# Kernel optimization log

Hardware: AMD Instinct MI355X
Metric: run time of the kernel (lower is better)

Reference implementation:

```python
import jax, jax.numpy as jnp
import numpy as np

B, S, D = 2, 2048, 3584
H, KV, HD = 28, 4, 128
N_REP = H // KV          # 7
MAX_S = 2048
SCALE = HD ** -0.5
ROPE_BASE = 1_000_000.0  # Qwen2 rope theta


def _rope_tables(max_s, hd, base):
    inv = 1.0 / (base ** (np.arange(0, hd, 2, dtype=np.float32) / hd))  # [hd/2]
    ang = np.arange(max_s, dtype=np.float32)[:, None] * inv[None, :]    # [S, hd/2]
    return jnp.asarray(np.cos(ang)), jnp.asarray(np.sin(ang))


def apply_rotary(x, cos, sin):
    # x: [b, s, h, hd] with interleaved complex pairs (torch view_as_complex layout)
    xr = x[..., 0::2]
    xi = x[..., 1::2]
    cos = cos[None, :, None, :]
    sin = sin[None, :, None, :]
    yr = xr * cos - xi * sin
    yi = xr * sin + xi * cos
    return jnp.stack([yr, yi], axis=-1).reshape(x.shape)


def setup_inputs() -> dict:
    key = jax.random.key(0)
    ks = jax.random.split(key, 8)
    w = 0.02
    x = jax.random.normal(ks[0], (B, S, D), jnp.float32)
    wq_w = jax.random.normal(ks[1], (H * HD, D), jnp.float32) * w
    wq_b = jax.random.normal(ks[2], (H * HD,), jnp.float32) * w
    wk_w = jax.random.normal(ks[3], (KV * HD, D), jnp.float32) * w
    wk_b = jax.random.normal(ks[4], (KV * HD,), jnp.float32) * w
    wv_w = jax.random.normal(ks[5], (KV * HD, D), jnp.float32) * w
    wv_b = jax.random.normal(ks[6], (KV * HD,), jnp.float32) * w
    wo_w = jax.random.normal(ks[7], (D, H * HD), jnp.float32) * w
    k_cache = jnp.zeros((B, MAX_S, KV, HD), jnp.float32)
    v_cache = jnp.zeros((B, MAX_S, KV, HD), jnp.float32)
    freqs_cos, freqs_sin = _rope_tables(MAX_S, HD, ROPE_BASE)
    # causal additive mask [s, t]; large-negative instead of -inf for safe grads
    mask = jnp.triu(jnp.full((S, S), -1e9, jnp.float32), k=1)
    return {"x": x, "wq_w": wq_w, "wq_b": wq_b, "wk_w": wk_w, "wk_b": wk_b,
            "wv_w": wv_w, "wv_b": wv_b, "wo_w": wo_w,
            "k_cache": k_cache, "v_cache": v_cache,
            "freqs_cos": freqs_cos, "freqs_sin": freqs_sin,
            "mask": mask, "start_pos": 0}


def reference(x, wq_w, wq_b, wk_w, wk_b, wv_w, wv_b, wo_w,
              k_cache, v_cache, freqs_cos, freqs_sin, mask, start_pos):
    bsz, seqlen, _ = x.shape
    end_pos = start_pos + seqlen
    q = (x @ wq_w.T + wq_b).reshape(bsz, seqlen, H, HD)
    k = (x @ wk_w.T + wk_b).reshape(bsz, seqlen, KV, HD)
    v = (x @ wv_w.T + wv_b).reshape(bsz, seqlen, KV, HD)
    cos = jax.lax.dynamic_slice_in_dim(freqs_cos, start_pos, seqlen, 0)
    sin = jax.lax.dynamic_slice_in_dim(freqs_sin, start_pos, seqlen, 0)
    q = apply_rotary(q, cos, sin)
    k = apply_rotary(k, cos, sin)
    # KV-cache write
    k_cache = jax.lax.dynamic_update_slice(k_cache, k, (0, start_pos, 0, 0))
    v_cache = jax.lax.dynamic_update_slice(v_cache, v, (0, start_pos, 0, 0))
    keys = k_cache[:bsz, :end_pos]    # [b, t, kv, hd]
    values = v_cache[:bsz, :end_pos]
    # GQA: repeat_interleave kv heads to n_heads
    keys = jnp.repeat(keys, N_REP, axis=2)      # [b, t, h, hd]
    values = jnp.repeat(values, N_REP, axis=2)
    scores = jnp.einsum('bshd,bthd->bsht', q, keys) * SCALE
    scores = scores + mask[None, :, None, :]
    probs = jax.nn.softmax(scores.astype(jnp.float32), axis=-1).astype(x.dtype)
    out = jnp.einsum('bsht,bthd->bshd', probs, values)
    out = out.reshape(bsz, seqlen, H * HD)
    return out @ wo_w.T
```

## Files before the change

kernel.cpp:

```cpp
#include <hip/hip_runtime.h>
#include <hip/hip_bf16.h>

typedef __attribute__((ext_vector_type(4)))  float  f32x4;
typedef __attribute__((ext_vector_type(16))) float  f32x16;
typedef __attribute__((ext_vector_type(8)))  __bf16 bf16x8;
typedef __attribute__((ext_vector_type(4)))  __bf16 bf16x4;
typedef __attribute__((ext_vector_type(4)))  unsigned int u32x4;

constexpr int S_LEN = 2048, DMODEL = 3584, NH = 28, NKV = 4, HD = 128, NREP = 7;
constexpr float SCALE_LOG2 = 0.1275174331f;

__device__ __forceinline__ unsigned int pack2(float a, float b) {
  unsigned short ua = __builtin_bit_cast(unsigned short, (__bf16)a);
  unsigned short ub = __builtin_bit_cast(unsigned short, (__bf16)b);
  return (unsigned int)ua | ((unsigned int)ub << 16);
}

__global__ void cvt5_kernel(const float* __restrict__ s0, const float* __restrict__ s1,
                            const float* __restrict__ s2, const float* __restrict__ s3,
                            const float* __restrict__ s4,
                            __bf16* __restrict__ d0, __bf16* __restrict__ d1,
                            __bf16* __restrict__ d2, __bf16* __restrict__ d3,
                            __bf16* __restrict__ d4,
                            int n0, int n1, int n2, int n3, int* __restrict__ ctr, int total) {
  if (blockIdx.x == 0 && threadIdx.x == 0) *ctr = 0;
  for (int i = blockIdx.x * blockDim.x + threadIdx.x; i < total; i += gridDim.x * blockDim.x) {
    const float* s; __bf16* d; int j = i;
    if (j < n0) { s = s0; d = d0; }
    else { j -= n0;
      if (j < n1) { s = s1; d = d1; }
      else { j -= n1;
        if (j < n2) { s = s2; d = d2; }
        else { j -= n2;
          if (j < n3) { s = s3; d = d3; }
          else { j -= n3; s = s4; d = d4; }
        }
      }
    }
    float4 v = reinterpret_cast<const float4*>(s)[j];
    bf16x4 o;
    o[0] = (__bf16)v.x; o[1] = (__bf16)v.y; o[2] = (__bf16)v.z; o[3] = (__bf16)v.w;
    reinterpret_cast<bf16x4*>(d)[j] = o;
  }
}

#define GLDS16(gsrc, ldst)                                                              \
  __builtin_amdgcn_global_load_lds((const __attribute__((address_space(1))) void*)(gsrc),\
                                   (__attribute__((address_space(3))) void*)(ldst), 16, 0, 0)

template <int MODE>
__global__ __launch_bounds__(512, 4) void gemm256(
    const __bf16* __restrict__ A, const __bf16* __restrict__ Bw,
    const float* __restrict__ bias, void* __restrict__ Cout,
    int M, int N, int K,
    const float* __restrict__ fcos, const float* __restrict__ fsin,
    const int* __restrict__ sp_ptr, float scale)
{
  extern __shared__ char smem[];
  const int tid = threadIdx.x;
  const int lane = tid & 63, wid = tid >> 6;
  const int wm = wid >> 2, wn = wid & 3;
  const int l15 = lane & 15, g = (lane >> 4) & 3;

  const int chunk = gridDim.x >> 3;
  const int wg = (blockIdx.x & 7) * chunk + (blockIdx.x >> 3);
  const int nbx = N >> 8;
  const int by = wg / nbx, bx = wg % nbx;
  const int row0 = by * 128, col0 = bx * 256;

  const int srL   = 16 * (tid >> 6) + ((tid >> 2) & 15);
  const int cperm = ((tid & 3) * 8) ^ (((tid >> 5) & 1) * 16);
  const __bf16* pA  = A + (size_t)(row0 + srL) * K + cperm;
  const __bf16* pB0 = Bw + (size_t)(col0 + srL) * K + cperm;
  const __bf16* pB1 = pB0 + (size_t)128 * K;
  char* ldsD = smem + tid * 16;

  const int sw  = ((l15 >> 3) & 1) << 5;
  const int rdo = l15 * 64 + ((g * 16) ^ sw);
  const int aoff = wm * 4096 + rdo;
  int bofs[4];
#pragma unroll
  for (int fn = 0; fn < 4; fn++) {
    const int c = wn * 64 + fn * 16;
    bofs[fn] = 8192 + (c >> 7) * 8192 + ((c >> 4) & 7) * 1024 + rdo;
  }

  f32x4 acc[4][4] = {};
  const int nt = K >> 5;

#pragma unroll
  for (int pt = 0; pt < 2; pt++) {
    const size_t ko = (size_t)pt * 32;
    char* base = ldsD + pt * 24576;
    GLDS16(pA + ko, base);
    GLDS16(pB0 + ko, base + 8192);
    GLDS16(pB1 + ko, base + 16384);
  }
  asm volatile("s_waitcnt vmcnt(3)" ::: "memory");
  __builtin_amdgcn_s_barrier();
  __builtin_amdgcn_sched_barrier(0);

  int sl = 0, sl2 = 2;
  for (int t = 0; t < nt; t++) {
    const char* sb = smem + sl * 24576;
    bf16x8 af[4], bfv[4];

    bfv[0] = *reinterpret_cast<const bf16x8*>(sb + bofs[0]);
    bfv[1] = *reinterpret_cast<const bf16x8*>(sb + bofs[1]);
#pragma unroll
    for (int fm = 0; fm < 4; fm++)
      af[fm] = *reinterpret_cast<const bf16x8*>(sb + aoff + fm * 1024);
    __builtin_amdgcn_sched_barrier(0);
    bfv[2] = *reinterpret_cast<const bf16x8*>(sb + bofs[2]);
    bfv[3] = *reinterpret_cast<const bf16x8*>(sb + bofs[3]);

    if (t + 2 < nt) {
      const size_t ko = (size_t)(t + 2) * 32;
      char* base = ldsD + sl2 * 24576;
      GLDS16(pA + ko, base);
      GLDS16(pB0 + ko, base + 8192);
      GLDS16(pB1 + ko, base + 16384);
    }

    asm volatile("s_waitcnt lgkmcnt(2)" ::: "memory");
    __builtin_amdgcn_sched_barrier(0);
    __builtin_amdgcn_s_setprio(1);
#pragma unroll
    for (int fn = 0; fn < 2; fn++)
#pragma unroll
      for (int fm = 0; fm < 4; fm++)
        acc[fm][fn] = __builtin_amdgcn_mfma_f32_16x16x32_bf16(af[fm], bfv[fn], acc[fm][fn], 0, 0, 0);
    __builtin_amdgcn_s_setprio(0);

    asm volatile("s_waitcnt lgkmcnt(0)" ::: "memory");
    __builtin_amdgcn_sched_barrier(0);
    __builtin_amdgcn_s_setprio(1);
#pragma unroll
    for (int fn = 2; fn < 4; fn++)
#pragma unroll
      for (int fm = 0; fm < 4; fm++)
        acc[fm][fn] = __builtin_amdgcn_mfma_f32_16x16x32_bf16(af[fm], bfv[fn], acc[fm][fn], 0, 0, 0);
    __builtin_amdgcn_s_setprio(0);

    if (t < nt - 2)       asm volatile("s_waitcnt vmcnt(3)" ::: "memory");
    else if (t == nt - 2) asm volatile("s_waitcnt vmcnt(0)" ::: "memory");
    __builtin_amdgcn_s_barrier();
    __builtin_amdgcn_sched_barrier(0);

    sl = (sl == 2) ? 0 : sl + 1;
    sl2 = (sl2 == 2) ? 0 : sl2 + 1;
  }

  if constexpr (MODE == 0) {
    float* C = (float*)Cout;
#pragma unroll
    for (int fm = 0; fm < 4; fm++) {
      const int row = row0 + wm * 64 + fm * 16 + 4 * g;
#pragma unroll
      for (int fn = 0; fn < 4; fn++) {
        const int col = col0 + wn * 64 + fn * 16 + l15;
#pragma unroll
        for (int r = 0; r < 4; r++)
          C[(size_t)(row + r) * N + col] = acc[fm][fn][r];
      }
    }
  } else {
    __bf16* C = (__bf16*)Cout;
    const int sp = sp_ptr[0];
    float bval[4];
#pragma unroll
    for (int fn = 0; fn < 4; fn++) bval[fn] = bias[col0 + wn * 64 + fn * 16 + l15];
#pragma unroll
    for (int fm = 0; fm < 4; fm++) {
#pragma unroll
      for (int fn = 0; fn < 4; fn++) {
        const int col = col0 + wn * 64 + fn * 16 + l15;
        const int i = (col & (HD - 1)) >> 1;
#pragma unroll
        for (int r = 0; r < 4; r++) {
          const int row = row0 + wm * 64 + fm * 16 + 4 * g + r;
          float y = acc[fm][fn][r] + bval[fn];
          float p = __shfl_xor(y, 1);
          const int spos = sp + (row & (S_LEN - 1));
          const float c = fcos[spos * (HD / 2) + i];
          const float sn = fsin[spos * (HD / 2) + i];
          y = (col & 1) ? (p * sn + y * c) : (y * c - p * sn);
          C[(size_t)row * N + col] = (__bf16)(y * scale);
        }
      }
    }
  }
}

__global__ __launch_bounds__(256) void gemm_kv(
    const __bf16* __restrict__ A,
    const __bf16* __restrict__ Wk, const float* __restrict__ bk, __bf16* __restrict__ Ko,
    const __bf16* __restrict__ Wv, const float* __restrict__ bv, __bf16* __restrict__ Vt,
    const float* __restrict__ fcos, const float* __restrict__ fsin,
    const int* __restrict__ sp_ptr)
{
  constexpr int N = 512, K = 3584;
  __shared__ __bf16 As[128 * 32];
  __shared__ __bf16 Bs[128 * 32];
  const int tid = threadIdx.x;
  const int lane = tid & 63, wid = tid >> 6;
  const int l15 = lane & 15, g = lane >> 4;
  const int wr = wid >> 1, wc = wid & 1;
  const bool isK = blockIdx.x < 4;
  const __bf16* Bw = isK ? Wk : Wv;
  const float* bias = isK ? bk : bv;
  const int row0 = blockIdx.y * 128;
  const int col0 = (blockIdx.x & 3) * 128;

  f32x4 acc[4][4] = {};

  const int srow = tid >> 2;
  const int scol = (tid & 3) * 8;
  const __bf16* Ag0 = A + (size_t)(row0 + srow) * K + scol;
  const __bf16* Ag1 = Ag0 + (size_t)64 * K;
  const __bf16* Bg0 = Bw + (size_t)(col0 + srow) * K + scol;
  const __bf16* Bg1 = Bg0 + (size_t)64 * K;
  __bf16* As0 = As + tid * 8;
  __bf16* As1 = As + 2048 + tid * 8;
  __bf16* Bs0 = Bs + tid * 8;
  __bf16* Bs1 = Bs + 2048 + tid * 8;

  for (int k0 = 0; k0 < K; k0 += 32) {
    GLDS16(Ag0 + k0, As0);
    GLDS16(Ag1 + k0, As1);
    GLDS16(Bg0 + k0, Bs0);
    GLDS16(Bg1 + k0, Bs1);
    __syncthreads();
    bf16x8 af[4], bfr[4];
#pragma unroll
    for (int m = 0; m < 4; m++)
      af[m] = *reinterpret_cast<const bf16x8*>(As + (wr * 64 + m * 16 + l15) * 32 + g * 8);
#pragma unroll
    for (int n = 0; n < 4; n++)
      bfr[n] = *reinterpret_cast<const bf16x8*>(Bs + (wc * 64 + n * 16 + l15) * 32 + g * 8);
#pragma unroll
    for (int m = 0; m < 4; m++)
#pragma unroll
      for (int n = 0; n < 4; n++)
        acc[m][n] = __builtin_amdgcn_mfma_f32_16x16x32_bf16(af[m], bfr[n], acc[m][n], 0, 0, 0);
    __syncthreads();
  }

  const int sp = sp_ptr[0];
  if (isK) {
#pragma unroll
    for (int m = 0; m < 4; m++) {
#pragma unroll
      for (int n = 0; n < 4; n++) {
        const int col = col0 + wc * 64 + n * 16 + l15;
        const float bval = bias[col];
        f32x4 v = acc[m][n];
#pragma unroll
        for (int r = 0; r < 4; r++) {
          const int row = row0 + wr * 64 + m * 16 + 4 * g + r;
          float y = v[r] + bval;
          float p = __shfl_xor(y, 1);
          const int i = (col & (HD - 1)) >> 1;
          const int spos = sp + (row & (S_LEN - 1));
          const float c = fcos[spos * (HD / 2) + i];
          const float sn = fsin[spos * (HD / 2) + i];
          y = (col & 1) ? (p * sn + y * c) : (y * c - p * sn);
          Ko[(size_t)row * N + col] = (__bf16)y;
        }
      }
    }
  } else {
    const int b4kv = ((row0 >> 11) * 4) + (blockIdx.x & 3);
    __bf16* vbase = Vt + ((size_t)b4kv << 18);
#pragma unroll
    for (int m = 0; m < 4; m++) {
#pragma unroll
      for (int n = 0; n < 4; n++) {
        const int d = wc * 64 + n * 16 + l15;
        const float bval = bias[col0 + d];
        const int s0 = (row0 + wr * 64 + m * 16 + 4 * g) & (S_LEN - 1);
        f32x4 v = acc[m][n];
        bf16x4 o;
#pragma unroll
        for (int r = 0; r < 4; r++) o[r] = (__bf16)(v[r] + bval);
        *reinterpret_cast<bf16x4*>(vbase + (size_t)d * S_LEN + s0) = o;
      }
    }
  }
}

__global__ __launch_bounds__(256, 2) void attn_kernel(
    const __bf16* __restrict__ Qb, const __bf16* __restrict__ Kb,
    const __bf16* __restrict__ Vt, __bf16* __restrict__ Ob, int* __restrict__ ctr)
{
  __shared__ __align__(16) char asmem[65536];
  __shared__ int jsh;

  const int tid = threadIdx.x, lane = tid & 63, wid = tid >> 6;
  const int l31 = lane & 31, hh = lane >> 5;

  const int trow = tid >> 4;
  const int kcol = (((tid & 15) * 16) ^ ((trow & 7) << 4)) >> 1;
  const int vrow = tid >> 3;
  const int vcol = (((tid & 7) * 16) ^ ((vrow & 7) << 4)) >> 1;

  constexpr int NITEMS = 16 * NH * 2;

  while (true) {
    if (tid == 0) jsh = atomicAdd(ctr, 1);
    __syncthreads();
    const int j = jsh;
    if (j >= NITEMS) break;

    const int qi = 15 - (j / 56);
    const int r56 = j % 56;
    const int h = r56 >> 1, b = r56 & 1;
    const int kvh = h / NREP;
    const int qw = qi * 128 + wid * 32;
    const int qg = qw + l31;

    const __bf16* Kbase = Kb + ((size_t)b * S_LEN * NKV + kvh) * HD;
    const __bf16* Vbase = Vt + ((size_t)b * NKV + kvh) * (size_t)HD * S_LEN;

    bf16x8 qf[8];
    {
      const __bf16* qp = Qb + (((size_t)b * S_LEN + qg) * NH + h) * HD + hh * 8;
#pragma unroll
      for (int c = 0; c < 8; c++) qf[c] = *reinterpret_cast<const bf16x8*>(qp + c * 16);
    }

    f32x16 o[4] = {};
    float mrun = -3.0e38f, lsum = 0.0f;

    const int ntiles = 2 * qi + 2;

#define STAGE(T, S)                                                                     \
    do {                                                                                \
      const int k0_ = (T) * 64;                                                         \
      char* Kd_ = asmem + (S) * 32768;                                                  \
      char* Vd_ = Kd_ + 16384;                                                          \
      _Pragma("unroll")                                                                 \
      for (int p = 0; p < 4; p++) {                                                     \
        GLDS16(Kbase + (size_t)(k0_ + p * 16 + trow) * (NKV * HD) + kcol,               \
               Kd_ + (p * 256 + tid) * 16);                                             \
        GLDS16(Vbase + (size_t)(p * 32 + vrow) * S_LEN + k0_ + vcol,                    \
               Vd_ + (p * 256 + tid) * 16);                                             \
      }                                                                                 \
    } while (0)

    STAGE(0, 0);

    for (int t = 0; t < ntiles; t++) {
      __syncthreads();
      if (t + 1 < ntiles) STAGE(t + 1, (t + 1) & 1);

      const char* Ksb = asmem + (t & 1) * 32768;
      const char* Vsb = Ksb + 16384;
      const int k0 = t * 64;

      f32x16 s0 = {}, s1 = {};
      {
        const char* kp0 = Ksb + l31 * 256;
        const char* kp1 = kp0 + 32 * 256;
        const int sw = (l31 & 7) << 4;
        __builtin_amdgcn_s_setprio(1);
#pragma unroll
        for (int c = 0; c < 8; c++) {
          const int cb = (c * 32 + hh * 16) ^ sw;
          bf16x8 kf0 = *reinterpret_cast<const bf16x8*>(kp0 + cb);
          s0 = __builtin_amdgcn_mfma_f32_32x32x16_bf16(kf0, qf[c], s0, 0, 0, 0);
          bf16x8 kf1 = *reinterpret_cast<const bf16x8*>(kp1 + cb);
          s1 = __builtin_amdgcn_mfma_f32_32x32x16_bf16(kf1, qf[c], s1, 0, 0, 0);
        }
        __builtin_amdgcn_s_setprio(0);
      }

      if (k0 + 63 > qw) {
#pragma unroll
        for (int r = 0; r < 16; r++) {
          const int kvo = k0 + ((r & 3) + 8 * (r >> 2)) + 4 * hh;
          if (kvo > qg)      s0[r] = -1.0e9f;
          if (kvo + 32 > qg) s1[r] = -1.0e9f;
        }
      }

      float pmax = -3.0e38f;
#pragma unroll
      for (int r = 0; r < 16; r++) { pmax = fmaxf(pmax, s0[r]); pmax = fmaxf(pmax, s1[r]); }
      pmax = fmaxf(pmax, __shfl_xor(pmax, 32));
      if (!__all(pmax <= mrun + 11.5f)) {
        const float mnew = fmaxf(mrun, pmax);
        const float fs = exp2f(mrun - mnew);
        lsum *= fs;
#pragma unroll
        for (int dt = 0; dt < 4; dt++) o[dt] *= fs;
        mrun = mnew;
      }
      float psum = 0.0f;
#pragma unroll
      for (int r = 0; r < 16; r++) {
        s0[r] = exp2f(s0[r] - mrun); psum += s0[r];
        s1[r] = exp2f(s1[r] - mrun); psum += s1[r];
      }
      lsum += psum;

      unsigned int pk[2][8], px[2][8];
#pragma unroll
      for (int jj = 0; jj < 8; jj++) {
        pk[0][jj] = pack2(s0[2 * jj], s0[2 * jj + 1]);
        pk[1][jj] = pack2(s1[2 * jj], s1[2 * jj + 1]);
      }
#pragma unroll
      for (int tt = 0; tt < 2; tt++)
#pragma unroll
        for (int jj = 0; jj < 8; jj++) px[tt][jj] = __shfl_xor(pk[tt][jj], 32);

      __builtin_amdgcn_s_setprio(1);
#pragma unroll
      for (int tt = 0; tt < 2; tt++) {
#pragma unroll
        for (int c2 = 0; c2 < 2; c2++) {
          u32x4 pb4;
          if (hh == 0)
            pb4 = (u32x4){pk[tt][4 * c2], pk[tt][4 * c2 + 1], px[tt][4 * c2], px[tt][4 * c2 + 1]};
          else
            pb4 = (u32x4){px[tt][4 * c2 + 2], px[tt][4 * c2 + 3], pk[tt][4 * c2 + 2], pk[tt][4 * c2 + 3]};
          bf16x8 pbf = __builtin_bit_cast(bf16x8, pb4);
          const int colb = tt * 64 + c2 * 32 + hh * 16;
#pragma unroll
          for (int dt = 0; dt < 4; dt++) {
            const int d = dt * 32 + l31;
            bf16x8 vf = *reinterpret_cast<const bf16x8*>(Vsb + d * 128 + (colb ^ ((d & 7) << 4)));
            o[dt] = __builtin_amdgcn_mfma_f32_32x32x16_bf16(vf, pbf, o[dt], 0, 0, 0);
          }
        }
      }
      __builtin_amdgcn_s_setprio(0);
    }
#undef STAGE

    lsum += __shfl_xor(lsum, 32);
    const float inv = 1.0f / lsum;
    char* my = asmem + wid * 8192;
#pragma unroll
    for (int dt = 0; dt < 4; dt++) {
#pragma unroll
      for (int jj = 0; jj < 8; jj++) {
        const int r = 2 * jj;
        const int d = dt * 32 + ((r & 3) + 8 * (r >> 2)) + 4 * hh;
        const unsigned int w = pack2(o[dt][r] * inv, o[dt][r + 1] * inv);
        *reinterpret_cast<unsigned int*>(my + ((l31 * 256 + d * 2) ^ ((l31 & 7) << 4))) = w;
      }
    }
#pragma unroll
    for (int jj = 0; jj < 8; jj++) {
      const int idx = jj * 64 + lane;
      const int row = idx >> 4, c16 = idx & 15;
      u32x4 val = *reinterpret_cast<u32x4*>(my + row * 256 + ((c16 * 16) ^ ((row & 7) << 4)));
      *reinterpret_cast<u32x4*>(Ob + (size_t)(b * S_LEN + qw + row) * (NH * HD) + h * HD + c16 * 8) = val;
    }
  }
}

extern "C" void kernel_launch(void* const* d_in, const int* in_sizes, int n_in,
                              void* d_out, int out_size, void* d_ws, size_t ws_size,
                              hipStream_t stream) {
  (void)in_sizes; (void)n_in; (void)out_size; (void)ws_size;
  const float* x    = (const float*)d_in[0];
  const float* wq_w = (const float*)d_in[1];
  const float* wq_b = (const float*)d_in[2];
  const float* wk_w = (const float*)d_in[3];
  const float* wk_b = (const float*)d_in[4];
  const float* wv_w = (const float*)d_in[5];
  const float* wv_b = (const float*)d_in[6];
  const float* wo_w = (const float*)d_in[7];
  const float* fcos = (const float*)d_in[10];
  const float* fsin = (const float*)d_in[11];
  const int*   spp  = (const int*)d_in[13];
  float* out = (float*)d_out;

  constexpr size_t XB_N = (size_t)4096 * 3584;
  constexpr size_t WQ_N = (size_t)3584 * 3584;
  constexpr size_t WK_N = (size_t)512 * 3584;
  constexpr size_t WO_N = (size_t)3584 * 3584;
  constexpr size_t KB_N = (size_t)4096 * 512;

  __bf16* xb  = (__bf16*)d_ws;
  __bf16* wqb = xb + XB_N;
  __bf16* wkb = wqb + WQ_N;
  __bf16* wvb = wkb + WK_N;
  __bf16* wob = wvb + WK_N;
  __bf16* Qb  = wob + WO_N;
  __bf16* Kb  = Qb + XB_N;
  __bf16* Vt  = Kb + KB_N;
  int*    ctr = (int*)(Vt + KB_N);
  __bf16* Ob  = xb;

  constexpr int N0 = (int)(XB_N / 4), N1 = (int)(WQ_N / 4), N2 = (int)(WK_N / 4),
                N3 = (int)(WK_N / 4), N4 = (int)(WO_N / 4);
  constexpr int NTOT = N0 + N1 + N2 + N3 + N4;
  cvt5_kernel<<<2048, 256, 0, stream>>>(x, wq_w, wk_w, wv_w, wo_w,
                                        xb, wqb, wkb, wvb, wob,
                                        N0, N1, N2, N3, ctr, NTOT);

  gemm256<2><<<dim3(448), 512, 73728, stream>>>(xb, wqb, wq_b, Qb, 4096, 3584, 3584,
                                                fcos, fsin, spp, SCALE_LOG2);
  gemm_kv<<<dim3(8, 32), 256, 0, stream>>>(xb, wkb, wk_b, Kb, wvb, wv_b, Vt,
                                           fcos, fsin, spp);
  attn_kernel<<<dim3(512), 256, 0, stream>>>(Qb, Kb, Vt, Ob, ctr);
  gemm256<0><<<dim3(448), 512, 73728, stream>>>(Ob, wob, nullptr, out, 4096, 3584, 3584,
                                                nullptr, nullptr, nullptr, 1.0f);
}
```

Baseline: 455.4 us.

## Enlarge GEMM tile to 256x256 with B fragments loaded directly into registers

The Q and output projection GEMMs move from 128x256 to 256x256 tiles, so each wave computes 8x4 MFMA fragments and the grid is halved to 224 workgroups. The weight (B) operand no longer goes through LDS. Each lane loads its B fragments straight from global memory into double-buffered registers, while A uses a 4-slot LDS ring with 3-deep prefetch. This aims to cut LDS traffic and raise arithmetic intensity per tile. The costs are higher register pressure (launch bounds lowered to 2 blocks per SM), fewer workgroups than the 256 CUs, and uncoalesced per-lane global loads for B.

```diff
diff --git a/kernel.cpp b/kernel.cpp
--- a/kernel.cpp
+++ b/kernel.cpp
@@ -49,7 +49,7 @@
                                    (__attribute__((address_space(3))) void*)(ldst), 16, 0, 0)
 
 template <int MODE>
-__global__ __launch_bounds__(512, 4) void gemm256(
+__global__ __launch_bounds__(512, 2) void gemm256(
     const __bf16* __restrict__ A, const __bf16* __restrict__ Bw,
     const float* __restrict__ bias, void* __restrict__ Cout,
     int M, int N, int K,
@@ -66,96 +66,100 @@
   const int wg = (blockIdx.x & 7) * chunk + (blockIdx.x >> 3);
   const int nbx = N >> 8;
   const int by = wg / nbx, bx = wg % nbx;
-  const int row0 = by * 128, col0 = bx * 256;
+  const int row0 = by * 256, col0 = bx * 256;
 
   const int srL   = 16 * (tid >> 6) + ((tid >> 2) & 15);
   const int cperm = ((tid & 3) * 8) ^ (((tid >> 5) & 1) * 16);
-  const __bf16* pA  = A + (size_t)(row0 + srL) * K + cperm;
-  const __bf16* pB0 = Bw + (size_t)(col0 + srL) * K + cperm;
-  const __bf16* pB1 = pB0 + (size_t)128 * K;
-  char* ldsD = smem + tid * 16;
-
-  const int sw  = ((l15 >> 3) & 1) << 5;
-  const int rdo = l15 * 64 + ((g * 16) ^ sw);
-  const int aoff = wm * 4096 + rdo;
-  int bofs[4];
-#pragma unroll
-  for (int fn = 0; fn < 4; fn++) {
-    const int c = wn * 64 + fn * 16;
-    bofs[fn] = 8192 + (c >> 7) * 8192 + ((c >> 4) & 7) * 1024 + rdo;
-  }
-
-  f32x4 acc[4][4] = {};
+  const __bf16* pA0 = A + (size_t)(row0 + srL) * K + cperm;
+  const __bf16* pA1 = pA0 + (size_t)128 * K;
+  char* ldsA = smem + tid * 16;
+
+  const int sw = ((l15 >> 3) & 1) << 5;
+  const int aoff = wm * 8192 + l15 * 64 + ((g * 16) ^ sw);
+
+  const __bf16* pBf[4];
+#pragma unroll
+  for (int fn = 0; fn < 4; fn++)
+    pBf[fn] = Bw + (size_t)(col0 + wn * 64 + fn * 16 + l15) * K + g * 8;
+
+  f32x4 acc[8][4] = {};
   const int nt = K >> 5;
-
-#pragma unroll
-  for (int pt = 0; pt < 2; pt++) {
-    const size_t ko = (size_t)pt * 32;
-    char* base = ldsD + pt * 24576;
-    GLDS16(pA + ko, base);
-    GLDS16(pB0 + ko, base + 8192);
-    GLDS16(pB1 + ko, base + 16384);
-  }
-  asm volatile("s_waitcnt vmcnt(3)" ::: "memory");
+  bf16x8 bE[4], bO[4];
+
+#pragma unroll
+  for (int pt = 0; pt < 3; pt++) {
+    char* sA = ldsA + pt * 16384;
+    GLDS16(pA0 + (size_t)pt * 32, sA);
+    GLDS16(pA1 + (size_t)pt * 32, sA + 8192);
+  }
+  __builtin_amdgcn_sched_barrier(0);
+#pragma unroll
+  for (int fn = 0; fn < 4; fn++) bE[fn] = *reinterpret_cast<const bf16x8*>(pBf[fn]);
+#pragma unroll
+  for (int fn = 0; fn < 4; fn++) bO[fn] = *reinterpret_cast<const bf16x8*>(pBf[fn] + 32);
+  asm volatile("s_waitcnt vmcnt(12)" ::: "memory");
   __builtin_amdgcn_s_barrier();
   __builtin_amdgcn_sched_barrier(0);
 
-  int sl = 0, sl2 = 2;
-  for (int t = 0; t < nt; t++) {
-    const char* sb = smem + sl * 24576;
-    bf16x8 af[4], bfv[4];
-
-    bfv[0] = *reinterpret_cast<const bf16x8*>(sb + bofs[0]);
-    bfv[1] = *reinterpret_cast<const bf16x8*>(sb + bofs[1]);
-#pragma unroll
-    for (int fm = 0; fm < 4; fm++)
-      af[fm] = *reinterpret_cast<const bf16x8*>(sb + aoff + fm * 1024);
-    __builtin_amdgcn_sched_barrier(0);
-    bfv[2] = *reinterpret_cast<const bf16x8*>(sb + bofs[2]);
-    bfv[3] = *reinterpret_cast<const bf16x8*>(sb + bofs[3]);
-
-    if (t + 2 < nt) {
-      const size_t ko = (size_t)(t + 2) * 32;
-      char* base = ldsD + sl2 * 24576;
-      GLDS16(pA + ko, base);
-      GLDS16(pB0 + ko, base + 8192);
-      GLDS16(pB1 + ko, base + 16384);
-    }
-
-    asm volatile("s_waitcnt lgkmcnt(2)" ::: "memory");
-    __builtin_amdgcn_sched_barrier(0);
-    __builtin_amdgcn_s_setprio(1);
-#pragma unroll
-    for (int fn = 0; fn < 2; fn++)
-#pragma unroll
-      for (int fm = 0; fm < 4; fm++)
-        acc[fm][fn] = __builtin_amdgcn_mfma_f32_16x16x32_bf16(af[fm], bfv[fn], acc[fm][fn], 0, 0, 0);
-    __builtin_amdgcn_s_setprio(0);
-
-    asm volatile("s_waitcnt lgkmcnt(0)" ::: "memory");
-    __builtin_amdgcn_sched_barrier(0);
-    __builtin_amdgcn_s_setprio(1);
-#pragma unroll
-    for (int fn = 2; fn < 4; fn++)
-#pragma unroll
-      for (int fm = 0; fm < 4; fm++)
-        acc[fm][fn] = __builtin_amdgcn_mfma_f32_16x16x32_bf16(af[fm], bfv[fn], acc[fm][fn], 0, 0, 0);
-    __builtin_amdgcn_s_setprio(0);
-
-    if (t < nt - 2)       asm volatile("s_waitcnt vmcnt(3)" ::: "memory");
-    else if (t == nt - 2) asm volatile("s_waitcnt vmcnt(0)" ::: "memory");
-    __builtin_amdgcn_s_barrier();
-    __builtin_amdgcn_sched_barrier(0);
-
-    sl = (sl == 2) ? 0 : sl + 1;
-    sl2 = (sl2 == 2) ? 0 : sl2 + 1;
-  }
+#define TILE(T, BR)                                                                     \
+  do {                                                                                  \
+    const int slot = ((T) & 3) * 16384;                                                 \
+    const char* sa = smem + slot + aoff;                                                \
+    bf16x8 a0[4], a1[4];                                                                \
+    _Pragma("unroll")                                                                   \
+    for (int fm = 0; fm < 4; fm++)                                                      \
+      a0[fm] = *reinterpret_cast<const bf16x8*>(sa + fm * 1024);                        \
+    _Pragma("unroll")                                                                   \
+    for (int fm = 0; fm < 4; fm++)                                                      \
+      a1[fm] = *reinterpret_cast<const bf16x8*>(sa + (4 + fm) * 1024);                  \
+                         \
+    if ((T) == 0)            asm volatile("s_waitcnt vmcnt(4) lgkmcnt(0)" ::: "memory");\
+    else if ((T) <= nt - 3)  asm volatile("s_waitcnt vmcnt(6) lgkmcnt(0)" ::: "memory");\
+    else if ((T) == nt - 2)  asm volatile("s_waitcnt vmcnt(4) lgkmcnt(0)" ::: "memory");\
+    else                     asm volatile("s_waitcnt vmcnt(0) lgkmcnt(0)" ::: "memory");\
+    __builtin_amdgcn_sched_barrier(0);                                                  \
+    __builtin_amdgcn_s_setprio(1);                                                      \
+    _Pragma("unroll")                                                                   \
+    for (int fn = 0; fn < 4; fn++)                                                      \
+      _Pragma("unroll")                                                                 \
+      for (int fm = 0; fm < 4; fm++)                                                    \
+        acc[fm][fn] = __builtin_amdgcn_mfma_f32_16x16x32_bf16(a0[fm], BR[fn],           \
+                                                              acc[fm][fn], 0, 0, 0);   \
+    _Pragma("unroll")                                                                   \
+    for (int fn = 0; fn < 4; fn++)                                                      \
+      _Pragma("unroll")                                                                 \
+      for (int fm = 0; fm < 4; fm++)                                                    \
+        acc[4 + fm][fn] = __builtin_amdgcn_mfma_f32_16x16x32_bf16(a1[fm], BR[fn],       \
+                                                                  acc[4 + fm][fn],     \
+                                                                  0, 0, 0);            \
+    __builtin_amdgcn_s_setprio(0);                                                      \
+    __builtin_amdgcn_sched_barrier(0);                                                  \
+                \
+    if ((T) + 3 < nt) {                                                                 \
+      char* sA = ldsA + (((T) + 3) & 3) * 16384;                                        \
+      GLDS16(pA0 + (size_t)((T) + 3) * 32, sA);                                         \
+      GLDS16(pA1 + (size_t)((T) + 3) * 32, sA + 8192);                                  \
+    }                                                                                   \
+    if ((T) + 2 < nt) {                                                                 \
+      _Pragma("unroll")                                                                 \
+      for (int fn = 0; fn < 4; fn++)                                                    \
+        BR[fn] = *reinterpret_cast<const bf16x8*>(pBf[fn] + (size_t)((T) + 2) * 32);    \
+    }                                                                                   \
+    __builtin_amdgcn_s_barrier();                                                       \
+    __builtin_amdgcn_sched_barrier(0);                                                  \
+  } while (0)
+
+  for (int t = 0; t < nt; t += 2) {
+    TILE(t, bE);
+    TILE(t + 1, bO);
+  }
+#undef TILE
 
   if constexpr (MODE == 0) {
     float* C = (float*)Cout;
 #pragma unroll
-    for (int fm = 0; fm < 4; fm++) {
-      const int row = row0 + wm * 64 + fm * 16 + 4 * g;
+    for (int fm = 0; fm < 8; fm++) {
+      const int row = row0 + wm * 128 + fm * 16 + 4 * g;
 #pragma unroll
       for (int fn = 0; fn < 4; fn++) {
         const int col = col0 + wn * 64 + fn * 16 + l15;
@@ -171,14 +175,14 @@
 #pragma unroll
     for (int fn = 0; fn < 4; fn++) bval[fn] = bias[col0 + wn * 64 + fn * 16 + l15];
 #pragma unroll
-    for (int fm = 0; fm < 4; fm++) {
+    for (int fm = 0; fm < 8; fm++) {
 #pragma unroll
       for (int fn = 0; fn < 4; fn++) {
         const int col = col0 + wn * 64 + fn * 16 + l15;
         const int i = (col & (HD - 1)) >> 1;
 #pragma unroll
         for (int r = 0; r < 4; r++) {
-          const int row = row0 + wm * 64 + fm * 16 + 4 * g + r;
+          const int row = row0 + wm * 128 + fm * 16 + 4 * g + r;
           float y = acc[fm][fn][r] + bval[fn];
           float p = __shfl_xor(y, 1);
           const int spos = sp + (row & (S_LEN - 1));
@@ -503,11 +507,11 @@
                                         xb, wqb, wkb, wvb, wob,
                                         N0, N1, N2, N3, ctr, NTOT);
 
-  gemm256<2><<<dim3(448), 512, 73728, stream>>>(xb, wqb, wq_b, Qb, 4096, 3584, 3584,
+  gemm256<2><<<dim3(224), 512, 65536, stream>>>(xb, wqb, wq_b, Qb, 4096, 3584, 3584,
                                                 fcos, fsin, spp, SCALE_LOG2);
   gemm_kv<<<dim3(8, 32), 256, 0, stream>>>(xb, wkb, wk_b, Kb, wvb, wv_b, Vt,
                                            fcos, fsin, spp);
   attn_kernel<<<dim3(512), 256, 0, stream>>>(Qb, Kb, Vt, Ob, ctr);
-  gemm256<0><<<dim3(448), 512, 73728, stream>>>(Ob, wob, nullptr, out, 4096, 3584, 3584,
+  gemm256<0><<<dim3(224), 512, 65536, stream>>>(Ob, wob, nullptr, out, 4096, 3584, 3584,
                                                 nullptr, nullptr, nullptr, 1.0f);
 }
```

Result: slower. 484.3 us (+6.4%).
